# Kernel optimization log

Measured on AMD Instinct MI355X. Metric: run time of the kernel, lower is better.

The kernel has to match this reference:

```python
import jax, jax.numpy as jnp
import numpy as np

# MoE config (mirrors init_kwargs)
E = 8        # num_experts
K = 2        # num_experts_per_tok
H = 1024     # hidden_size
F = 2816     # moe_intermediate_size
B, S = 2, 512
NORM_TOPK = True


def setup_inputs() -> dict:
    key = jax.random.key(0)
    ks = jax.random.split(key, 5)
    x = jax.random.normal(ks[0], (B, S, H), dtype=jnp.float32)
    router_w = jax.random.normal(ks[1], (E, H), dtype=jnp.float32) * 0.02   # nn.Linear(H, E).weight
    gate_proj = jax.random.normal(ks[2], (E, H, F), dtype=jnp.float32) * 0.02
    up_proj = jax.random.normal(ks[3], (E, H, F), dtype=jnp.float32) * 0.02
    down_proj = jax.random.normal(ks[4], (E, F, H), dtype=jnp.float32) * 0.02
    return {"x": x, "router_w": router_w, "gate_proj": gate_proj,
            "up_proj": up_proj, "down_proj": down_proj}


def reference(x, router_w, gate_proj, up_proj, down_proj):
    b, s, h = x.shape
    xf = x.reshape(-1, h)                                    # [T, H]
    # Router: softmax over experts, top-k selection mask
    logits = xf @ router_w.T                                 # [T, E]
    probs = jax.nn.softmax(logits, axis=-1)
    topk_p, topk_i = jax.lax.top_k(probs, K)                 # [T, K]
    routing_map = jax.nn.one_hot(topk_i, E, dtype=probs.dtype).sum(axis=1)  # [T, E] 0/1
    if NORM_TOPK:
        probs = probs / topk_p.sum(-1, keepdims=True)
    weight = probs * routing_map                             # [T, E]; zero for unselected experts
    # Per-expert SwiGLU FFN; combine weighted by routing prob.
    # Dense-masked formulation: mathematically identical to the original
    # gather -> per-expert GEMM -> scatter_add, since weight==0 for unrouted pairs.
    g = jnp.einsum('th,ehf->tef', xf, gate_proj)             # [T, E, F]
    u = jnp.einsum('th,ehf->tef', xf, up_proj)               # [T, E, F]
    m = jax.nn.silu(g) * u                                   # [T, E, F]
    out = jnp.einsum('tef,efh,te->th', m, down_proj, weight) # [T, H]
    return out.reshape(b, s, h)
```

## Files before the change

### kernel.cpp

```cpp
#include <hip/hip_runtime.h>

#define HD 1024
#define FD 2816
#define NE 8
#define NT 1024
#define NSLOT (NT * 2)

typedef short short8 __attribute__((ext_vector_type(8)));
typedef unsigned u32x4 __attribute__((ext_vector_type(4)));
typedef unsigned u32x2 __attribute__((ext_vector_type(2)));
typedef float f32x4 __attribute__((ext_vector_type(4)));
typedef float f32x16 __attribute__((ext_vector_type(16)));

typedef __attribute__((address_space(3))) unsigned lds_u32;
typedef __attribute__((address_space(1))) const unsigned glb_u32;

#define WAITV(N) asm volatile("s_waitcnt vmcnt(" #N ") lgkmcnt(0)" ::: "memory")
#define BARRIER() do { __builtin_amdgcn_s_barrier(); __builtin_amdgcn_sched_barrier(0); } while (0)
#define SB() __builtin_amdgcn_sched_barrier(0)

__device__ __forceinline__ void glds16(const void* g, void* l) {
  __builtin_amdgcn_global_load_lds((glb_u32*)g, (lds_u32*)l, 16, 0, 0);
}

__device__ __forceinline__ short f2bf(float f) {
  unsigned u = __builtin_bit_cast(unsigned, f);
  u += 0x7FFFu + ((u >> 16) & 1u);
  return (short)(u >> 16);
}
__device__ __forceinline__ unsigned cvtpk(float lo, float hi) {
  unsigned r;
  asm("v_cvt_pk_bf16_f32 %0, %1, %2" : "=v"(r) : "v"(lo), "v"(hi));
  return r;
}
__device__ __forceinline__ int imin(int a, int b) { return a < b ? a : b; }

__global__ void router_kernel(const float* __restrict__ x,
                              const float* __restrict__ rw,
                              int* __restrict__ counts,
                              int* __restrict__ tok_i,
                              float* __restrict__ tok_w) {
  const int t = blockIdx.x;
  const int lane = threadIdx.x;
  const float* px = x + (size_t)t * HD;
  float acc[NE];
#pragma unroll
  for (int e = 0; e < NE; e++) acc[e] = 0.f;
  for (int h = lane; h < HD; h += 64) {
    float xv = px[h];
#pragma unroll
    for (int e = 0; e < NE; e++) acc[e] += xv * rw[e * HD + h];
  }
#pragma unroll
  for (int e = 0; e < NE; e++) {
#pragma unroll
    for (int off = 32; off > 0; off >>= 1)
      acc[e] += __shfl_xor(acc[e], off, 64);
  }
  if (lane == 0) {
    float mx = acc[0];
#pragma unroll
    for (int e = 1; e < NE; e++) mx = fmaxf(mx, acc[e]);
    float ex[NE];
#pragma unroll
    for (int e = 0; e < NE; e++) ex[e] = __expf(acc[e] - mx);
    int i1 = 0;
#pragma unroll
    for (int e = 1; e < NE; e++) if (ex[e] > ex[i1]) i1 = e;
    int i2 = (i1 == 0) ? 1 : 0;
#pragma unroll
    for (int e = 0; e < NE; e++) if (e != i1 && ex[e] > ex[i2]) i2 = e;
    float inv = 1.f / (ex[i1] + ex[i2]);
    tok_i[t * 2 + 0] = i1; tok_w[t * 2 + 0] = ex[i1] * inv;
    tok_i[t * 2 + 1] = i2; tok_w[t * 2 + 1] = ex[i2] * inv;
    atomicAdd(&counts[i1], 1);
    atomicAdd(&counts[i2], 1);
  }
}

__global__ void scanfill_kernel(const int* __restrict__ counts,
                                const int* __restrict__ tok_i,
                                const float* __restrict__ tok_w,
                                int* __restrict__ bases,
                                int* __restrict__ slot_token,
                                float* __restrict__ slot_w) {
  __shared__ int cur[NE];
  const int t = threadIdx.x;
  if (t == 0) {
    int s = 0;
    for (int e = 0; e < NE; e++) { bases[e] = s; cur[e] = s; s += counts[e]; }
    bases[NE] = s;
  }
  __syncthreads();
#pragma unroll
  for (int k = 0; k < 2; k++) {
    int e = tok_i[t * 2 + k];
    int pos = atomicAdd(&cur[e], 1);
    slot_token[pos] = t;
    slot_w[pos] = tok_w[t * 2 + k];
  }
}

__device__ __forceinline__ void pack_block(const float* __restrict__ W,
                                           short* __restrict__ P, int K, int N,
                                           int f0, int kt, int e, int tid,
                                           char* smem) {
  const int KT = K >> 5;
  const int lane = tid & 63, w = tid >> 6;
  const float* src = W + (size_t)e * K * N + (size_t)(kt * 32 + w * 8) * N +
                     f0 + lane * 4;
  f32x4 x0 = *(const f32x4*)(src);
  f32x4 x1 = *(const f32x4*)(src + (size_t)N);
  f32x4 x2 = *(const f32x4*)(src + (size_t)2 * N);
  f32x4 x3 = *(const f32x4*)(src + (size_t)3 * N);
  f32x4 x4 = *(const f32x4*)(src + (size_t)4 * N);
  f32x4 x5 = *(const f32x4*)(src + (size_t)5 * N);
  f32x4 x6 = *(const f32x4*)(src + (size_t)6 * N);
  f32x4 x7 = *(const f32x4*)(src + (size_t)7 * N);
  unsigned* Lb = (unsigned*)(smem + w * 4608);
#pragma unroll
  for (int j = 0; j < 4; j++) {
    u32x4 c;
    c[0] = cvtpk(x0[j], x1[j]);
    c[1] = cvtpk(x2[j], x3[j]);
    c[2] = cvtpk(x4[j], x5[j]);
    c[3] = cvtpk(x6[j], x7[j]);
    int ch = 4 * lane + j;
    *(u32x4*)(Lb + (ch + (ch >> 3)) * 4) = c;
  }
  asm volatile("s_waitcnt lgkmcnt(0)" ::: "memory");
  SB();
  short* dstb = P + (((size_t)(e * KT + kt) * 4 + w) * N + f0) * 8;
#pragma unroll
  for (int j = 0; j < 4; j++) {
    int ch = j * 64 + lane;
    u32x4 c = *(const u32x4*)(Lb + (ch + (ch >> 3)) * 4);
    *(u32x4*)(dstb + (size_t)ch * 8) = c;
  }
}

__global__ __launch_bounds__(256, 4) void pack_gu_gather_kernel(
    const float* __restrict__ gw, const float* __restrict__ uw,
    short* __restrict__ Pg, short* __restrict__ Pu,
    const float* __restrict__ x, const int* __restrict__ slot_token,
    short* __restrict__ xg) {
  __shared__ char smem[18432];
  const int bid = blockIdx.x;
  const int tid = threadIdx.x;
  if (bid < 5632) {
    const int f0 = (bid % 11) * 256;
    const int kt = (bid / 11) % 32;
    const int ez = bid / 352;
    pack_block(ez < NE ? gw : uw, ez < NE ? Pg : Pu, HD, FD, f0, kt, ez & 7,
               tid, smem);
  } else {
    const int slot = bid - 5632;
    const int tok = slot_token[slot];
    f32x4 v = *(const f32x4*)(x + (size_t)tok * HD + tid * 4);
    u32x2 s;
    s[0] = cvtpk(v[0], v[1]);
    s[1] = cvtpk(v[2], v[3]);
    *(u32x2*)&xg[(size_t)slot * HD + tid * 4] = s;
  }
}


#define G_STAGE(S, T) do {                                           \
    glds16(asrc0 + (T) * 32, &As[S][wid * 512]);                     \
    glds16(asrc1 + (T) * 32, &As[S][2048 + wid * 512]);              \
    glds16(bgsrc + (size_t)(T) * 90112, &Bg[S][wid * 512]);          \
    glds16(busrc + (size_t)(T) * 90112, &Bu[S][wid * 512]);          \
  } while (0)

#define G_COMPUTE(S) do {                                                     \
    _Pragma("unroll")                                                         \
    for (int ks = 0; ks < 2; ks++) {                                          \
      const int oct = ks * 2 + l5;                                            \
      short8 a0, a1, bg, bu;                                                  \
      { int r = wm * 64 + l31, p = r >> 1;                                    \
        a0 = *(const short8*)&As[S][p * 64 +                                  \
              ((((r & 1) << 2) | oct) ^ (p & 7)) * 8]; }                      \
      { int r = wm * 64 + 32 + l31, p = r >> 1;                               \
        a1 = *(const short8*)&As[S][p * 64 +                                  \
              ((((r & 1) << 2) | oct) ^ (p & 7)) * 8]; }                      \
      { int n = wn * 32 + l31, pn = n >> 1;                                   \
        int off = pn * 64 + ((((n & 1) << 2) | oct) ^ (pn & 7)) * 8;          \
        bg = *(const short8*)&Bg[S][off];                                     \
        bu = *(const short8*)&Bu[S][off]; }                                   \
      accG0 = __builtin_amdgcn_mfma_f32_32x32x16_bf16(a0, bg, accG0, 0, 0, 0);\
      accU0 = __builtin_amdgcn_mfma_f32_32x32x16_bf16(a0, bu, accU0, 0, 0, 0);\
      accG1 = __builtin_amdgcn_mfma_f32_32x32x16_bf16(a1, bg, accG1, 0, 0, 0);\
      accU1 = __builtin_amdgcn_mfma_f32_32x32x16_bf16(a1, bu, accU1, 0, 0, 0);\
    }                                                                         \
  } while (0)

#define G_ITER(S, T) do {    \
    G_COMPUTE(S);            \
    BARRIER();               \
    G_STAGE(S, (T) + 3);     \
    WAITV(8);                \
    BARRIER();               \
  } while (0)

__global__ __launch_bounds__(256, 3) void gemm_gu_packd_kernel(
    const short* __restrict__ xg, const short* __restrict__ Pg,
    const short* __restrict__ Pu, const int* __restrict__ bases,
    short* __restrict__ m_out, const float* __restrict__ dw,
    short* __restrict__ Pd, int gemmN) {
  __shared__ char smem[49152];
  const int bid = blockIdx.x;
  const int tid = threadIdx.x;

  if (bid >= gemmN) {
    const int pid = bid - gemmN;
    const int f0 = (pid & 3) * 256;
    const int kt = (pid >> 2) % 88;
    const int e = pid / 352;
    pack_block(dw, Pd, FD, HD, f0, kt, e, tid, smem);
    return;
  }

  const int gx = bid % 352;
  const int e = gx / 44, nt = gx - e * 44;
  const int b0 = bases[e];
  const int ne = bases[e + 1] - b0;
  const int row0 = (bid / 352) * 128;
  if (row0 >= ne) return;
  const int n0 = nt * 64;

  short (*As)[4096] = (short(*)[4096])smem;
  short (*Bg)[2048] = (short(*)[2048])(smem + 24576);
  short (*Bu)[2048] = (short(*)[2048])(smem + 36864);

  const int lane = tid & 63, wid = tid >> 6;
  const int l31 = lane & 31, l5 = lane >> 5;
  const int wm = wid >> 1, wn = wid & 1;

  const short *asrc0, *asrc1;
  {
    int i = tid;
    int p = i >> 3, j = i & 7, v = j ^ (p & 7);
    int r = 2 * p + (v >> 2), c = v & 3;
    asrc0 = xg + (size_t)(b0 + imin(row0 + r, ne - 1)) * HD + c * 8;
    i = 256 + tid;
    p = i >> 3; j = i & 7; v = j ^ (p & 7);
    r = 2 * p + (v >> 2); c = v & 3;
    asrc1 = xg + (size_t)(b0 + imin(row0 + r, ne - 1)) * HD + c * 8;
  }
  const short *bgsrc, *busrc;
  {
    int p = tid >> 3, j = tid & 7, v = j ^ (p & 7);
    int r = 2 * p + (v >> 2), c = v & 3;
    size_t off = ((size_t)(e * 32 * 4 + c)) * (FD * 8) + (size_t)(n0 + r) * 8;
    bgsrc = Pg + off;
    busrc = Pu + off;
  }

  f32x16 accG0 = (f32x16)0.f, accG1 = (f32x16)0.f;
  f32x16 accU0 = (f32x16)0.f, accU1 = (f32x16)0.f;

  G_STAGE(0, 0); G_STAGE(1, 1); G_STAGE(2, 2);
  WAITV(8);
  BARRIER();

  for (int t = 0; t < 27; t += 3) {
    G_ITER(0, t);
    G_ITER(1, t + 1);
    G_ITER(2, t + 2);
  }
  G_ITER(0, 27);
  G_ITER(1, 28);
  G_COMPUTE(2);
  WAITV(4); BARRIER();
  G_COMPUTE(0);
  WAITV(0); BARRIER();
  G_COMPUTE(1);

#pragma unroll
  for (int q = 0; q < 16; q++) {
    int rb_ = (q & 3) + 8 * (q >> 2) + 4 * l5;
    {
      int r = row0 + wm * 64 + rb_;
      if (r < ne) {
        float g = accG0[q], u = accU0[q];
        float mv = (g / (1.f + __expf(-g))) * u;
        m_out[(size_t)(b0 + r) * FD + n0 + wn * 32 + l31] = f2bf(mv);
      }
    }
    {
      int r = row0 + wm * 64 + 32 + rb_;
      if (r < ne) {
        float g = accG1[q], u = accU1[q];
        float mv = (g / (1.f + __expf(-g))) * u;
        m_out[(size_t)(b0 + r) * FD + n0 + wn * 32 + l31] = f2bf(mv);
      }
    }
  }
}


#define D_STAGE(S, T) do {                                           \
    glds16(asrcA0 + (T) * 64, &As[S][wid * 512]);                    \
    glds16(asrcA1 + (T) * 64, &As[S][2048 + wid * 512]);             \
    glds16(bsrc0 + (size_t)(T) * 65536, &Bs[S][wid * 512]);          \
    glds16(bsrc1 + (size_t)(T) * 65536, &Bs[S][2048 + wid * 512]);   \
  } while (0)

#define D_COMPUTE(S) do {                                                     \
    _Pragma("unroll")                                                         \
    for (int ks = 0; ks < 4; ks++) {                                          \
      const int sub = ks >> 1, oct = (ks & 1) * 2 + l5;                       \
      short8 a, b;                                                            \
      { int r = wm * 32 + l31, p = r >> 1;                                    \
        a = *(const short8*)&As[S][sub * 2048 + p * 64 +                      \
              ((((r & 1) << 2) | oct) ^ (p & 7)) * 8]; }                      \
      { int n = wn * 32 + l31, pn = n >> 1;                                   \
        b = *(const short8*)&Bs[S][sub * 2048 + pn * 64 +                     \
              ((((n & 1) << 2) | oct) ^ (pn & 7)) * 8]; }                     \
      acc = __builtin_amdgcn_mfma_f32_32x32x16_bf16(a, b, acc, 0, 0, 0);      \
    }                                                                         \
  } while (0)

#define D_ITER(S, T) do {    \
    D_COMPUTE(S);            \
    BARRIER();               \
    D_STAGE(S, (T) + 3);     \
    WAITV(8);                \
    BARRIER();               \
  } while (0)

__global__ __launch_bounds__(256, 3) void down_kernel(
    const short* __restrict__ m_in, const short* __restrict__ Pd,
    const int* __restrict__ bases, const float* __restrict__ slot_w,
    const int* __restrict__ slot_token, float* __restrict__ out) {
  const int bx = blockIdx.x;
  const int e = bx >> 4, nt = bx & 15;
  const int b0 = bases[e];
  const int ne = bases[e + 1] - b0;
  const int row0 = blockIdx.y * 64;
  if (row0 >= ne) return;
  const int n0 = nt * 64;

  __shared__ short As[3][4096];
  __shared__ short Bs[3][4096];

  const int tid = threadIdx.x;
  const int lane = tid & 63, wid = tid >> 6;
  const int l31 = lane & 31, l5 = lane >> 5;
  const int wm = wid >> 1, wn = wid & 1;

  const short *asrcA0, *asrcA1;
  {
    int p = tid >> 3, j = tid & 7, v = j ^ (p & 7);
    int r = 2 * p + (v >> 2), c = v & 3;
    const short* base = m_in + (size_t)(b0 + imin(row0 + r, ne - 1)) * FD;
    asrcA0 = base + c * 8;
    asrcA1 = base + 32 + c * 8;
  }
  const short *bsrc0, *bsrc1;
  {
    int p = tid >> 3, j = tid & 7, v = j ^ (p & 7);
    int r = 2 * p + (v >> 2), c = v & 3;
    bsrc0 = Pd + ((size_t)((e * 88 + 0) * 4 + c)) * (HD * 8) + (size_t)(n0 + r) * 8;
    bsrc1 = Pd + ((size_t)((e * 88 + 1) * 4 + c)) * (HD * 8) + (size_t)(n0 + r) * 8;
  }

  f32x16 acc = (f32x16)0.f;

  D_STAGE(0, 0); D_STAGE(1, 1); D_STAGE(2, 2);
  WAITV(8);
  BARRIER();

  for (int t = 0; t < 39; t += 3) {
    D_ITER(0, t);
    D_ITER(1, t + 1);
    D_ITER(2, t + 2);
  }
  D_ITER(0, 39);
  D_ITER(1, 40);
  D_COMPUTE(2);
  WAITV(4); BARRIER();
  D_COMPUTE(0);
  WAITV(0); BARRIER();
  D_COMPUTE(1);

#pragma unroll
  for (int q = 0; q < 16; q++) {
    int r = row0 + wm * 32 + (q & 3) + 8 * (q >> 2) + 4 * l5;
    if (r < ne) {
      int slot = b0 + r;
      int tok = slot_token[slot];
      atomicAdd(&out[(size_t)tok * HD + n0 + wn * 32 + l31],
                acc[q] * slot_w[slot]);
    }
  }
}

extern "C" void kernel_launch(void* const* d_in, const int* in_sizes, int n_in,
                              void* d_out, int out_size, void* d_ws,
                              size_t ws_size, hipStream_t stream) {
  const float* x = (const float*)d_in[0];
  const float* rw = (const float*)d_in[1];
  const float* gw = (const float*)d_in[2];
  const float* uw = (const float*)d_in[3];
  const float* dw = (const float*)d_in[4];
  float* out = (float*)d_out;

  char* ws = (char*)d_ws;
  int* counts = (int*)(ws + 0);
  int* bases = (int*)(ws + 128);
  int* tok_i = (int*)(ws + 256);
  float* tok_w = (float*)(ws + 8448);
  int* slot_token = (int*)(ws + 16640);
  float* slot_w = (float*)(ws + 24832);
  short* xg = (short*)(ws + 41216);
  short* m  = (short*)(ws + 4235520);
  short* Pg = (short*)(ws + 15769856);
  short* Pu = (short*)(ws + 61907200);
  short* PdBig = (short*)(ws + 108044544);
  const bool big = ws_size >= (size_t)108044544 + 46137344;
  short* Pd = big ? PdBig : Pg;

  (void)hipMemsetAsync(counts, 0, 64, stream);
  (void)hipMemsetAsync(out, 0, (size_t)out_size * 4, stream);
  router_kernel<<<NT, 64, 0, stream>>>(x, rw, counts, tok_i, tok_w);
  scanfill_kernel<<<1, 1024, 0, stream>>>(counts, tok_i, tok_w, bases,
                                          slot_token, slot_w);
  pack_gu_gather_kernel<<<7680, 256, 0, stream>>>(gw, uw, Pg, Pu, x,
                                                  slot_token, xg);
  if (big) {
    gemm_gu_packd_kernel<<<5632 + 2816, 256, 0, stream>>>(
        xg, Pg, Pu, bases, m, dw, Pd, 5632);
  } else {
    gemm_gu_packd_kernel<<<5632, 256, 0, stream>>>(xg, Pg, Pu, bases, m, dw,
                                                   Pd, 5632);
    gemm_gu_packd_kernel<<<2816, 256, 0, stream>>>(xg, Pg, Pu, bases, m, dw,
                                                   Pd, 0);
  }
  down_kernel<<<dim3(128, 32), 256, 0, stream>>>(m, Pd, bases, slot_w,
                                                 slot_token, out);
}
```

Measured before the change: 198.8 us.

## Move down-weight packing into aux kernel and double down GEMM row tile

The down-projection weight packing moves out of the gate/up GEMM launch and into the aux packing kernel. That kernel now packs gate, up and down weights and gathers tokens in one launch, leaving the GEMM kernel with static shared memory and no packing branch. The down kernel tile grows from 64 to 128 rows, with two accumulators per wave reusing each B fragment. This halves B reloads and the row-tile grid, at the cost of more LDS per block, lower occupancy (launch bound 2) and fewer blocks for short experts.

```diff
diff --git a/kernel.cpp b/kernel.cpp
--- a/kernel.cpp
+++ b/kernel.cpp
@@ -139,22 +139,29 @@
   }
 }
 
-__global__ __launch_bounds__(256, 4) void pack_gu_gather_kernel(
+__global__ __launch_bounds__(256, 4) void aux_kernel(
     const float* __restrict__ gw, const float* __restrict__ uw,
-    short* __restrict__ Pg, short* __restrict__ Pu,
+    const float* __restrict__ dwv, short* __restrict__ Pg,
+    short* __restrict__ Pu, short* __restrict__ Pd,
     const float* __restrict__ x, const int* __restrict__ slot_token,
-    short* __restrict__ xg) {
+    short* __restrict__ xg, int pguN, int pdN) {
   __shared__ char smem[18432];
   const int bid = blockIdx.x;
   const int tid = threadIdx.x;
-  if (bid < 5632) {
+  if (bid < pguN) {
     const int f0 = (bid % 11) * 256;
     const int kt = (bid / 11) % 32;
     const int ez = bid / 352;
     pack_block(ez < NE ? gw : uw, ez < NE ? Pg : Pu, HD, FD, f0, kt, ez & 7,
                tid, smem);
+  } else if (bid < pguN + pdN) {
+    const int pid = bid - pguN;
+    const int f0 = (pid & 3) * 256;
+    const int kt = (pid >> 2) % 88;
+    const int e = pid / 352;
+    pack_block(dwv, Pd, FD, HD, f0, kt, e, tid, smem);
   } else {
-    const int slot = bid - 5632;
+    const int slot = bid - pguN - pdN;
     const int tok = slot_token[slot];
     f32x4 v = *(const f32x4*)(x + (size_t)tok * HD + tid * 4);
     u32x2 s;
@@ -202,24 +209,12 @@
     BARRIER();               \
   } while (0)
 
-__global__ __launch_bounds__(256, 3) void gemm_gu_packd_kernel(
+__global__ __launch_bounds__(256, 3) void gemm_gu_kernel(
     const short* __restrict__ xg, const short* __restrict__ Pg,
     const short* __restrict__ Pu, const int* __restrict__ bases,
-    short* __restrict__ m_out, const float* __restrict__ dw,
-    short* __restrict__ Pd, int gemmN) {
-  __shared__ char smem[49152];
+    short* __restrict__ m_out) {
   const int bid = blockIdx.x;
   const int tid = threadIdx.x;
-
-  if (bid >= gemmN) {
-    const int pid = bid - gemmN;
-    const int f0 = (pid & 3) * 256;
-    const int kt = (pid >> 2) % 88;
-    const int e = pid / 352;
-    pack_block(dw, Pd, FD, HD, f0, kt, e, tid, smem);
-    return;
-  }
-
   const int gx = bid % 352;
   const int e = gx / 44, nt = gx - e * 44;
   const int b0 = bases[e];
@@ -228,9 +223,9 @@
   if (row0 >= ne) return;
   const int n0 = nt * 64;
 
-  short (*As)[4096] = (short(*)[4096])smem;
-  short (*Bg)[2048] = (short(*)[2048])(smem + 24576);
-  short (*Bu)[2048] = (short(*)[2048])(smem + 36864);
+  __shared__ short As[3][4096];
+  __shared__ short Bg[3][2048];
+  __shared__ short Bu[3][2048];
 
   const int lane = tid & 63, wid = tid >> 6;
   const int l31 = lane & 31, l5 = lane >> 5;
@@ -300,8 +295,10 @@
 
 
 #define D_STAGE(S, T) do {                                           \
-    glds16(asrcA0 + (T) * 64, &As[S][wid * 512]);                    \
-    glds16(asrcA1 + (T) * 64, &As[S][2048 + wid * 512]);             \
+    glds16(asrcA[0] + (T) * 64, &As[S][wid * 512]);                  \
+    glds16(asrcA[1] + (T) * 64, &As[S][2048 + wid * 512]);           \
+    glds16(asrcA[2] + (T) * 64, &As[S][4096 + wid * 512]);           \
+    glds16(asrcA[3] + (T) * 64, &As[S][6144 + wid * 512]);           \
     glds16(bsrc0 + (size_t)(T) * 65536, &Bs[S][wid * 512]);          \
     glds16(bsrc1 + (size_t)(T) * 65536, &Bs[S][2048 + wid * 512]);   \
   } while (0)
@@ -310,14 +307,18 @@
     _Pragma("unroll")                                                         \
     for (int ks = 0; ks < 4; ks++) {                                          \
       const int sub = ks >> 1, oct = (ks & 1) * 2 + l5;                       \
-      short8 a, b;                                                            \
-      { int r = wm * 32 + l31, p = r >> 1;                                    \
-        a = *(const short8*)&As[S][sub * 2048 + p * 64 +                      \
+      short8 a0, a1, b;                                                       \
+      { int r = wm * 64 + l31, p = r >> 1;                                    \
+        a0 = *(const short8*)&As[S][sub * 4096 + p * 64 +                     \
+              ((((r & 1) << 2) | oct) ^ (p & 7)) * 8]; }                      \
+      { int r = wm * 64 + 32 + l31, p = r >> 1;                               \
+        a1 = *(const short8*)&As[S][sub * 4096 + p * 64 +                     \
               ((((r & 1) << 2) | oct) ^ (p & 7)) * 8]; }                      \
       { int n = wn * 32 + l31, pn = n >> 1;                                   \
         b = *(const short8*)&Bs[S][sub * 2048 + pn * 64 +                     \
               ((((n & 1) << 2) | oct) ^ (pn & 7)) * 8]; }                     \
-      acc = __builtin_amdgcn_mfma_f32_32x32x16_bf16(a, b, acc, 0, 0, 0);      \
+      acc0 = __builtin_amdgcn_mfma_f32_32x32x16_bf16(a0, b, acc0, 0, 0, 0);   \
+      acc1 = __builtin_amdgcn_mfma_f32_32x32x16_bf16(a1, b, acc1, 0, 0, 0);   \
     }                                                                         \
   } while (0)
 
@@ -325,11 +326,11 @@
     D_COMPUTE(S);            \
     BARRIER();               \
     D_STAGE(S, (T) + 3);     \
-    WAITV(8);                \
+    WAITV(12);               \
     BARRIER();               \
   } while (0)
 
-__global__ __launch_bounds__(256, 3) void down_kernel(
+__global__ __launch_bounds__(256, 2) void down_kernel(
     const short* __restrict__ m_in, const short* __restrict__ Pd,
     const int* __restrict__ bases, const float* __restrict__ slot_w,
     const int* __restrict__ slot_token, float* __restrict__ out) {
@@ -337,11 +338,11 @@
   const int e = bx >> 4, nt = bx & 15;
   const int b0 = bases[e];
   const int ne = bases[e + 1] - b0;
-  const int row0 = blockIdx.y * 64;
+  const int row0 = blockIdx.y * 128;
   if (row0 >= ne) return;
   const int n0 = nt * 64;
 
-  __shared__ short As[3][4096];
+  __shared__ short As[3][8192];
   __shared__ short Bs[3][4096];
 
   const int tid = threadIdx.x;
@@ -349,13 +350,15 @@
   const int l31 = lane & 31, l5 = lane >> 5;
   const int wm = wid >> 1, wn = wid & 1;
 
-  const short *asrcA0, *asrcA1;
-  {
-    int p = tid >> 3, j = tid & 7, v = j ^ (p & 7);
+  const short* asrcA[4];
+#pragma unroll
+  for (int q = 0; q < 4; q++) {
+    int i = q * 256 + tid;
+    int sub = i >> 9, ci = i & 511;
+    int p = ci >> 3, j = ci & 7, v = j ^ (p & 7);
     int r = 2 * p + (v >> 2), c = v & 3;
-    const short* base = m_in + (size_t)(b0 + imin(row0 + r, ne - 1)) * FD;
-    asrcA0 = base + c * 8;
-    asrcA1 = base + 32 + c * 8;
+    asrcA[q] = m_in + (size_t)(b0 + imin(row0 + r, ne - 1)) * FD + sub * 32 +
+               c * 8;
   }
   const short *bsrc0, *bsrc1;
   {
@@ -365,10 +368,10 @@
     bsrc1 = Pd + ((size_t)((e * 88 + 1) * 4 + c)) * (HD * 8) + (size_t)(n0 + r) * 8;
   }
 
-  f32x16 acc = (f32x16)0.f;
+  f32x16 acc0 = (f32x16)0.f, acc1 = (f32x16)0.f;
 
   D_STAGE(0, 0); D_STAGE(1, 1); D_STAGE(2, 2);
-  WAITV(8);
+  WAITV(12);
   BARRIER();
 
   for (int t = 0; t < 39; t += 3) {
@@ -379,19 +382,29 @@
   D_ITER(0, 39);
   D_ITER(1, 40);
   D_COMPUTE(2);
-  WAITV(4); BARRIER();
+  WAITV(6); BARRIER();
   D_COMPUTE(0);
   WAITV(0); BARRIER();
   D_COMPUTE(1);
 
 #pragma unroll
   for (int q = 0; q < 16; q++) {
-    int r = row0 + wm * 32 + (q & 3) + 8 * (q >> 2) + 4 * l5;
-    if (r < ne) {
-      int slot = b0 + r;
-      int tok = slot_token[slot];
-      atomicAdd(&out[(size_t)tok * HD + n0 + wn * 32 + l31],
-                acc[q] * slot_w[slot]);
+    int rb_ = (q & 3) + 8 * (q >> 2) + 4 * l5;
+    {
+      int r = row0 + wm * 64 + rb_;
+      if (r < ne) {
+        int slot = b0 + r;
+        atomicAdd(&out[(size_t)slot_token[slot] * HD + n0 + wn * 32 + l31],
+                  acc0[q] * slot_w[slot]);
+      }
+    }
+    {
+      int r = row0 + wm * 64 + 32 + rb_;
+      if (r < ne) {
+        int slot = b0 + r;
+        atomicAdd(&out[(size_t)slot_token[slot] * HD + n0 + wn * 32 + l31],
+                  acc1[q] * slot_w[slot]);
+      }
     }
   }
 }
@@ -426,17 +439,17 @@
   router_kernel<<<NT, 64, 0, stream>>>(x, rw, counts, tok_i, tok_w);
   scanfill_kernel<<<1, 1024, 0, stream>>>(counts, tok_i, tok_w, bases,
                                           slot_token, slot_w);
-  pack_gu_gather_kernel<<<7680, 256, 0, stream>>>(gw, uw, Pg, Pu, x,
-                                                  slot_token, xg);
   if (big) {
-    gemm_gu_packd_kernel<<<5632 + 2816, 256, 0, stream>>>(
-        xg, Pg, Pu, bases, m, dw, Pd, 5632);
+    aux_kernel<<<5632 + 2816 + 2048, 256, 0, stream>>>(
+        gw, uw, dw, Pg, Pu, Pd, x, slot_token, xg, 5632, 2816);
+    gemm_gu_kernel<<<352 * 8, 256, 0, stream>>>(xg, Pg, Pu, bases, m);
   } else {
-    gemm_gu_packd_kernel<<<5632, 256, 0, stream>>>(xg, Pg, Pu, bases, m, dw,
-                                                   Pd, 5632);
-    gemm_gu_packd_kernel<<<2816, 256, 0, stream>>>(xg, Pg, Pu, bases, m, dw,
-                                                   Pd, 0);
-  }
-  down_kernel<<<dim3(128, 32), 256, 0, stream>>>(m, Pd, bases, slot_w,
-                                                 slot_token, out);
-}
+    aux_kernel<<<5632 + 2048, 256, 0, stream>>>(
+        gw, uw, dw, Pg, Pu, Pd, x, slot_token, xg, 5632, 0);
+    gemm_gu_kernel<<<352 * 8, 256, 0, stream>>>(xg, Pg, Pu, bases, m);
+    aux_kernel<<<2816, 256, 0, stream>>>(gw, uw, dw, Pg, Pu, Pd, x,
+                                         slot_token, xg, 0, 2816);
+  }
+  down_kernel<<<dim3(128, 8), 256, 0, stream>>>(m, Pd, bases, slot_w,
+                                                slot_token, out);
+}
```

New measurement: 235.9 us. +18.7%, slower.
